# Optimization experiments

Hardware: AMD Instinct MI355X
Metric: run time of the kernel (lower is better)

The kernel has to match this reference:

```python
import jax, jax.numpy as jnp
import numpy as np


def setup_inputs() -> dict:
    key = jax.random.key(0)
    k1, k2 = jax.random.split(key)
    B, T, H, D = 2, 2048, 16, 64          # batch, seq, heads, head_dim
    NUM_HASHES, NUM_BUCKETS = 4, 64
    hidden_states = jax.random.normal(k1, (B, T, H * D), dtype=jnp.float32)
    # equivalent of torch.randn rotations with fixed hash_seed
    random_rotations = jax.random.normal(k2, (H, D, NUM_HASHES, NUM_BUCKETS // 2), dtype=jnp.float32)
    return {"hidden_states": hidden_states, "random_rotations": random_rotations}


def reference(hidden_states, random_rotations):
    # hidden_states: [B, T, H*D]; random_rotations: [H, D, num_hashes, num_buckets//2]
    H, D, num_hashes, half = random_rotations.shape
    B, T, _ = hidden_states.shape
    # _split_hidden_size_dim: [B,T,H*D] -> [B,H,T,D]
    v = hidden_states.reshape(B, T, H, D).transpose(0, 2, 1, 3)
    # rotated: [B, H, num_hashes, T, num_buckets//2]
    rotated = jnp.einsum('bhtd,hdnr->bhntr', v, random_rotations)
    rotated = jnp.concatenate([rotated, -rotated], axis=-1)  # [..., num_buckets]
    buckets = jnp.argmax(rotated, axis=-1)                   # [B, H, num_hashes, T]
    b = buckets.transpose(0, 1, 3, 2)                        # [B, H, T, num_hashes]
    # m[b,h,i,j] = any_n (bucket_n(i) == bucket_n(j)); OR-accumulate over the
    # small fixed num_hashes axis to avoid a [B,H,T,T,num_hashes] intermediate.
    m = jnp.zeros((B, H, T, T), dtype=bool)
    for n in range(num_hashes):
        bn = b[..., n]
        m = m | (bn[:, :, :, None] == bn[:, :, None, :])
    return m
```

## Files before the change

### kernel.cpp

```cpp
#include <hip/hip_runtime.h>
#include <stdint.h>

#define BB 2
#define HH 16
#define TT 2048
#define DD 64
#define NHASH 4
#define NHALF 32

__global__ __launch_bounds__(256, 3) void lsh_buckets_kernel(
    const float* __restrict__ hs,
    const float* __restrict__ rot,
    uint32_t* __restrict__ words)
{
    __shared__ uint32_t lds[12288];
    float4* v4 = (float4*)lds;
    float4* r4 = (float4*)(lds + 4096);

    const int blk  = blockIdx.x;
    const int bh   = blk >> 5;
    const int tblk = blk & 31;
    const int b    = bh >> 4;
    const int h    = bh & 15;
    const int t0   = tblk * 64;
    const int tid  = threadIdx.x;
    const int n    = tid >> 6;
    const int lane = tid & 63;
    const int tg   = lane >> 3;
    const int rg   = lane & 7;

    #pragma unroll
    for (int p = 0; p < 4; ++p) {
        const int k  = tid + p * 256;
        const int t  = k >> 4;
        const int d4 = k & 15;
        const float4 f = ((const float4*)(hs + ((size_t)(b * TT + t0 + t)) * (HH * DD) + h * DD))[d4];
        v4[t * 16 + (d4 ^ (t >> 3))] = f;
    }
    {
        const float* rh = rot + (size_t)h * (DD * NHASH * NHALF);
        float* rf = (float*)r4;
        #pragma unroll
        for (int p = 0; p < 32; ++p) {
            const int g  = tid + p * 256;
            const int d  = g >> 7;
            const int nr = g & 127;
            const int nn = nr >> 5;
            const int r  = nr & 31;
            const int slot = (d >> 2) ^ (r >> 2);
            rf[((nn * 32 + r) * 16 + slot) * 4 + (d & 3)] = rh[g];
        }
    }
    __syncthreads();

    double acc[8][4];
    #pragma unroll
    for (int i = 0; i < 8; ++i)
        #pragma unroll
        for (int j = 0; j < 4; ++j) acc[i][j] = 0.0;

    const int vbase = tg * 8 * 16;
    const int rbase = (n * 32 + rg * 4) * 16;

    for (int s = 0; s < 16; ++s) {
        double rd[4][4];
        #pragma unroll
        for (int j = 0; j < 4; ++j) {
            const float4 rf = r4[rbase + j * 16 + (s ^ rg)];
            rd[j][0] = (double)rf.x; rd[j][1] = (double)rf.y;
            rd[j][2] = (double)rf.z; rd[j][3] = (double)rf.w;
        }
        #pragma unroll
        for (int i = 0; i < 8; ++i) {
            const float4 vf = v4[vbase + i * 16 + (s ^ tg)];
            const double v0 = (double)vf.x, v1 = (double)vf.y;
            const double v2 = (double)vf.z, v3 = (double)vf.w;
            #pragma unroll
            for (int j = 0; j < 4; ++j) {
                acc[i][j] += v0 * rd[j][0];
                acc[i][j] += v1 * rd[j][1];
                acc[i][j] += v2 * rd[j][2];
                acc[i][j] += v3 * rd[j][3];
            }
        }
    }

    __syncthreads();
    float*    vmaxL = (float*)lds;
    float*    vminL = (float*)(lds + 2304);
    uint32_t* imaxL = lds + 4608;
    uint32_t* iminL = lds + 6912;
    uint32_t* bkt   = lds + 9216;

    #pragma unroll
    for (int i = 0; i < 8; ++i) {
        const int t = tg * 8 + i;
        float fmx = -INFINITY; int imx = 0;
        float fmn =  INFINITY; int imn = 0;
        #pragma unroll
        for (int j = 0; j < 4; ++j) {
            const float f = (float)acc[i][j];
            const int   r = rg * 4 + j;
            if (f > fmx) { fmx = f; imx = r; }
            if (f < fmn) { fmn = f; imn = r; }
        }
        const int o = (n * 64 + t) * 9 + rg;
        vmaxL[o] = fmx; vminL[o] = fmn;
        imaxL[o] = (uint32_t)imx; iminL[o] = (uint32_t)imn;
    }
    __syncthreads();
    {
        const int nn = tid >> 6;
        const int t  = tid & 63;
        float fmx = -INFINITY; int imx = 0;
        float fmn =  INFINITY; int imn = 0;
        #pragma unroll
        for (int g = 0; g < 8; ++g) {
            const int o = (nn * 64 + t) * 9 + g;
            const float fx = vmaxL[o];
            const float fn = vminL[o];
            if (fx > fmx) { fmx = fx; imx = (int)imaxL[o]; }
            if (fn < fmn) { fmn = fn; imn = (int)iminL[o]; }
        }
        const uint32_t bucket = (fmx >= -fmn) ? (uint32_t)imx : (uint32_t)(NHALF + imn);
        bkt[nn * 64 + t] = bucket;
    }
    __syncthreads();
    if (tid < 64) {
        words[(size_t)bh * TT + t0 + tid] = bkt[tid]
                                          | (bkt[64  + tid] << 8)
                                          | (bkt[128 + tid] << 16)
                                          | (bkt[192 + tid] << 24);
    }
}

#define ROWS 8
__device__ __forceinline__ uint32_t eq_any_byte(uint32_t a, uint32_t b) {
    const uint32_t x = a ^ b;
    return ((x - 0x01010101u) & ~x & 0x80808080u) ? 1u : 0u;
}

__global__ __launch_bounds__(256) void lsh_mask_kernel(
    const uint32_t* __restrict__ words,
    uint4* __restrict__ out)
{
    const int bh  = blockIdx.x >> 8;
    const int i0  = (blockIdx.x & 255) * ROWS;
    const int tid = threadIdx.x;
    const uint32_t* wrow = words + (bh << 11);

    const uint4 wj0 = ((const uint4*)wrow)[tid];
    const uint4 wj1 = ((const uint4*)wrow)[tid + 256];

    #pragma unroll
    for (int k = 0; k < ROWS; ++k) {
        const uint32_t wi = wrow[i0 + k];
        uint4 r0, r1;
        r0.x = eq_any_byte(wi, wj0.x); r0.y = eq_any_byte(wi, wj0.y);
        r0.z = eq_any_byte(wi, wj0.z); r0.w = eq_any_byte(wi, wj0.w);
        r1.x = eq_any_byte(wi, wj1.x); r1.y = eq_any_byte(wi, wj1.y);
        r1.z = eq_any_byte(wi, wj1.z); r1.w = eq_any_byte(wi, wj1.w);
        uint4* op = out + (((size_t)((bh << 11) + i0 + k)) << 9);
        op[tid]       = r0;
        op[tid + 256] = r1;
    }
}

extern "C" void kernel_launch(void* const* d_in, const int* in_sizes, int n_in,
                              void* d_out, int out_size, void* d_ws, size_t ws_size,
                              hipStream_t stream) {
    const float* hs  = (const float*)d_in[0];
    const float* rot = (const float*)d_in[1];
    uint32_t* words  = (uint32_t*)d_ws;

    lsh_buckets_kernel<<<BB * HH * (TT / 64), 256, 0, stream>>>(hs, rot, words);
    lsh_mask_kernel<<<BB * HH * (TT / ROWS), 256, 0, stream>>>(words, (uint4*)d_out);
}
```

Baseline: 134.2 us.

## Pre-transpose rotations in a separate kernel and write bucket bytes directly

Adds a small kernel that puts the rotation matrix into the swizzled float4 layout once, so each bucket block does 8 coalesced float4 copies into LDS instead of 32 scalar scattered stores. It also drops the final LDS staging and barrier by having each thread write its bucket byte straight to global memory. The cost is an extra kernel launch and byte-granular global stores.

```diff
diff --git a/kernel.cpp b/kernel.cpp
--- a/kernel.cpp
+++ b/kernel.cpp
@@ -8,9 +8,29 @@
 #define NHASH 4
 #define NHALF 32
 
+__global__ __launch_bounds__(256) void lsh_rot_transpose_kernel(
+    const float* __restrict__ rot,
+    float4* __restrict__ rot_t)
+{
+    const int h    = blockIdx.x >> 3;
+    const int part = blockIdx.x & 7;
+    const int k    = part * 256 + threadIdx.x;
+    const int nr   = k >> 4;
+    const int slot = k & 15;
+    const int r    = nr & 31;
+    const int d4   = slot ^ (r >> 2);
+    const float* rh = rot + (size_t)h * (DD * NHASH * NHALF);
+    float4 o;
+    o.x = rh[(d4 * 4 + 0) * 128 + nr];
+    o.y = rh[(d4 * 4 + 1) * 128 + nr];
+    o.z = rh[(d4 * 4 + 2) * 128 + nr];
+    o.w = rh[(d4 * 4 + 3) * 128 + nr];
+    rot_t[(size_t)h * 2048 + k] = o;
+}
+
 __global__ __launch_bounds__(256, 3) void lsh_buckets_kernel(
     const float* __restrict__ hs,
-    const float* __restrict__ rot,
+    const float4* __restrict__ rot_t,
     uint32_t* __restrict__ words)
 {
     __shared__ uint32_t lds[12288];
@@ -38,18 +58,10 @@
         v4[t * 16 + (d4 ^ (t >> 3))] = f;
     }
     {
-        const float* rh = rot + (size_t)h * (DD * NHASH * NHALF);
-        float* rf = (float*)r4;
+        const float4* rsrc = rot_t + (size_t)h * 2048;
         #pragma unroll
-        for (int p = 0; p < 32; ++p) {
-            const int g  = tid + p * 256;
-            const int d  = g >> 7;
-            const int nr = g & 127;
-            const int nn = nr >> 5;
-            const int r  = nr & 31;
-            const int slot = (d >> 2) ^ (r >> 2);
-            rf[((nn * 32 + r) * 16 + slot) * 4 + (d & 3)] = rh[g];
-        }
+        for (int p = 0; p < 8; ++p)
+            r4[tid + p * 256] = rsrc[tid + p * 256];
     }
     __syncthreads();
 
@@ -90,7 +102,6 @@
     float*    vminL = (float*)(lds + 2304);
     uint32_t* imaxL = lds + 4608;
     uint32_t* iminL = lds + 6912;
-    uint32_t* bkt   = lds + 9216;
 
     #pragma unroll
     for (int i = 0; i < 8; ++i) {
@@ -123,14 +134,7 @@
             if (fn < fmn) { fmn = fn; imn = (int)iminL[o]; }
         }
         const uint32_t bucket = (fmx >= -fmn) ? (uint32_t)imx : (uint32_t)(NHALF + imn);
-        bkt[nn * 64 + t] = bucket;
-    }
-    __syncthreads();
-    if (tid < 64) {
-        words[(size_t)bh * TT + t0 + tid] = bkt[tid]
-                                          | (bkt[64  + tid] << 8)
-                                          | (bkt[128 + tid] << 16)
-                                          | (bkt[192 + tid] << 24);
+        ((uint8_t*)words)[((size_t)bh * TT + t0 + t) * 4 + nn] = (uint8_t)bucket;
     }
 }
 
@@ -172,7 +176,9 @@
     const float* hs  = (const float*)d_in[0];
     const float* rot = (const float*)d_in[1];
     uint32_t* words  = (uint32_t*)d_ws;
+    float4*   rot_t  = (float4*)((uint8_t*)d_ws + 512 * 1024);
 
-    lsh_buckets_kernel<<<BB * HH * (TT / 64), 256, 0, stream>>>(hs, rot, words);
+    lsh_rot_transpose_kernel<<<128, 256, 0, stream>>>(rot, rot_t);
+    lsh_buckets_kernel<<<BB * HH * (TT / 64), 256, 0, stream>>>(hs, rot_t, words);
     lsh_mask_kernel<<<BB * HH * (TT / ROWS), 256, 0, stream>>>(words, (uint4*)d_out);
 }
```

Result: no change. 136.5 us (+1.8%).
